# Kernel optimization log

Measured on AMD Instinct MI355X. Metric: run time of the kernel, lower is better.

Reference implementation:

```python
import jax, jax.numpy as jnp
import numpy as np

N, C, H, W = 8, 256, 128, 128
HW = H * W
NB = 20            # boxes per image
TEMP = 0.5
RATIO = 1.0
IMG_H, IMG_W = 800.0, 800.0  # img_metas[i]['img_shape']


def setup_inputs() -> dict:
    key = jax.random.key(0)
    k1, k2, k3 = jax.random.split(key, 3)
    preds_S = jax.random.normal(k1, (HW, N, C), dtype=jnp.float32)
    preds_T = jax.random.normal(k2, (HW, N, C), dtype=jnp.float32)
    # boxes: random corner pairs in image coords, sorted so x1<=x2, y1<=y2
    u = jax.random.uniform(k3, (N, NB, 4), dtype=jnp.float32)
    x1 = jnp.minimum(u[..., 0], u[..., 2]) * IMG_W
    x2 = jnp.maximum(u[..., 0], u[..., 2]) * IMG_W
    y1 = jnp.minimum(u[..., 1], u[..., 3]) * IMG_H
    y2 = jnp.maximum(u[..., 1], u[..., 3]) * IMG_H
    gt_bboxes = jnp.stack([x1, y1, x2, y2], axis=-1)  # (N, NB, 4)
    return {"preds_S": preds_S, "preds_T": preds_T, "gt_bboxes": gt_bboxes}


def get_attention(preds, temp):
    # preds: (N, C, H, W)
    value = jnp.abs(preds)
    fea_map = value.mean(axis=1)                                   # (N, H, W)
    S_att = (H * W) * jax.nn.softmax((fea_map / temp).reshape(N, -1), axis=1)
    S_att = S_att.reshape(N, H, W)
    channel_map = value.mean(axis=(2, 3))                          # (N, C)
    C_att = C * jax.nn.softmax(channel_map / temp, axis=1)
    return S_att, C_att


def build_masks(gt_bboxes):
    # boxes scaled to feature grid (same math as torch loop, vectorized)
    wmin = jnp.floor(gt_bboxes[..., 0] / IMG_W * W).astype(jnp.int32)  # (N, NB)
    wmax = jnp.ceil(gt_bboxes[..., 2] / IMG_W * W).astype(jnp.int32)
    hmin = jnp.floor(gt_bboxes[..., 1] / IMG_H * H).astype(jnp.int32)
    hmax = jnp.ceil(gt_bboxes[..., 3] / IMG_H * H).astype(jnp.int32)
    area = 1.0 / (hmax + 1 - hmin).astype(jnp.float32) / (wmax + 1 - wmin).astype(jnp.float32)
    hh = jnp.arange(H)[None, None, :, None]
    ww = jnp.arange(W)[None, None, None, :]
    inside = ((hh >= hmin[:, :, None, None]) & (hh <= hmax[:, :, None, None]) &
              (ww >= wmin[:, :, None, None]) & (ww <= wmax[:, :, None, None]))  # (N, NB, H, W)
    # per-box max-scatter == max over boxes of (area where inside else 0)
    Mask_fg = jnp.max(jnp.where(inside, area[:, :, None, None], 0.0), axis=1)  # (N, H, W)
    Mask_bg = (Mask_fg <= 0).astype(jnp.float32)
    s = Mask_bg.sum(axis=(1, 2), keepdims=True)
    Mask_bg = jnp.where(s > 0, Mask_bg / s, Mask_bg)
    return Mask_fg, Mask_bg


def reference(preds_S, preds_T, gt_bboxes):
    # attention from DETACHED teacher features (preds_T.detach() in torch)
    pT_det = jax.lax.stop_gradient(preds_T)
    pT_new = pT_det.reshape(H, W, N, C).transpose(2, 3, 0, 1)  # (N, C, H, W)
    S_t, C_t = get_attention(pT_new, TEMP)

    Mask_fg, Mask_bg = build_masks(gt_bboxes)

    # flatten to the (HW, bs, .) layout of get_fea_loss
    flat = lambda m: m.transpose(1, 2, 0).reshape(HW, N, 1)
    S_t_f = flat(S_t)
    Mfg_f = flat(Mask_fg)
    Mbg_f = flat(Mask_bg)
    C_t_f = C_t[None]  # (1, bs, c) broadcast

    w = jnp.sqrt(S_t_f) * jnp.sqrt(C_t_f)
    fea_t = preds_T * w
    fea_s = preds_S * w
    diff = jnp.abs(fea_s - fea_t)
    fg_loss = jnp.sum(diff * jnp.sqrt(Mfg_f)) / HW
    bg_loss = jnp.sum(diff * jnp.sqrt(Mbg_f)) / HW
    return (fg_loss + bg_loss) * RATIO
```

## Files before the change

### kernel.cpp

```cpp
#include <hip/hip_runtime.h>

#define N_   8
#define C_   256
#define H_   128
#define W_   128
#define HW_  16384
#define NB_  20
constexpr float TEMP  = 0.5f;
constexpr float IMG_W = 800.0f;
constexpr float IMG_H = 800.0f;

using f4 = __attribute__((ext_vector_type(4))) float;

__device__ __forceinline__ float waveReduceSum(float v) {
    v += __shfl_xor(v, 32, 64);
    v += __shfl_xor(v, 16, 64);
    v += __shfl_xor(v, 8, 64);
    v += __shfl_xor(v, 4, 64);
    v += __shfl_xor(v, 2, 64);
    v += __shfl_xor(v, 1, 64);
    return v;
}

__global__ __launch_bounds__(256, 4) void k_stats(const float* __restrict__ pT,
                                                  float* __restrict__ chan_part,
                                                  float* __restrict__ fea_sum,
                                                  float* __restrict__ smax_part) {
    const int n     = blockIdx.x & 7;
    const int chunk = blockIdx.x >> 3;
    const int wave  = threadIdx.x >> 6;
    const int lane  = threadIdx.x & 63;
    const int hw0   = chunk * 64 + wave * 16;

    float4 cacc = make_float4(0.f, 0.f, 0.f, 0.f);
    float vmax = 0.f;
    #pragma unroll
    for (int g = 0; g < 4; ++g) {
        const int r = hw0 + g * 4;
        float p[4];
        #pragma unroll
        for (int j = 0; j < 4; ++j) {
            const float4 v = *(const float4*)(pT + ((size_t)((r + j) * N_ + n)) * C_ + lane * 4);
            const float ax = fabsf(v.x), ay = fabsf(v.y), az = fabsf(v.z), aw = fabsf(v.w);
            cacc.x += ax; cacc.y += ay; cacc.z += az; cacc.w += aw;
            p[j] = ax + ay + az + aw;
        }
        float a01 = (lane & 32) ? p[1] : p[0];
        float b01 = (lane & 32) ? p[0] : p[1];
        const float u01 = a01 + __shfl_xor(b01, 32, 64);
        float a23 = (lane & 32) ? p[3] : p[2];
        float b23 = (lane & 32) ? p[2] : p[3];
        const float u23 = a23 + __shfl_xor(b23, 32, 64);
        float aq = (lane & 16) ? u23 : u01;
        float bq = (lane & 16) ? u01 : u23;
        float u = aq + __shfl_xor(bq, 16, 64);
        u += __shfl_xor(u, 8, 64);
        u += __shfl_xor(u, 4, 64);
        u += __shfl_xor(u, 2, 64);
        u += __shfl_xor(u, 1, 64);
        vmax = fmaxf(vmax, u);
        if ((lane & 15) == 0) {
            const int q = lane >> 4;
            const int row = ((q & 1) << 1) | (q >> 1);
            fea_sum[n * HW_ + r + row] = u;
        }
    }
    vmax = fmaxf(vmax, __shfl_xor(vmax, 16, 64));
    vmax = fmaxf(vmax, __shfl_xor(vmax, 32, 64));

    __shared__ float lds[4][C_];
    __shared__ float wmax[4];
    if (lane == 0) wmax[wave] = vmax;
    ((float4*)lds[wave])[lane] = cacc;
    __syncthreads();
    const int c = threadIdx.x;
    chan_part[((size_t)(n * 256 + chunk)) * C_ + c] =
        lds[0][c] + lds[1][c] + lds[2][c] + lds[3][c];
    if (threadIdx.x == 0)
        smax_part[n * 256 + chunk] =
            fmaxf(fmaxf(wmax[0], wmax[1]), fmaxf(wmax[2], wmax[3]));
}

__global__ __launch_bounds__(256) void k_prep(const float* __restrict__ fea_sum,
                                              const float* __restrict__ chan_part,
                                              const float* __restrict__ smax_part,
                                              const float* __restrict__ gt,
                                              float* __restrict__ A_t,
                                              float* __restrict__ B) {
    const int n   = blockIdx.x >> 3;
    const int sub = blockIdx.x & 7;
    const int tid = threadIdx.x;
    __shared__ float red[256];
    __shared__ int   bb[NB_][4];
    __shared__ float barea[NB_];

    if (tid < NB_) {
        const float* bx = gt + ((size_t)n * NB_ + tid) * 4;
        const int wmin = (int)floorf(bx[0] / IMG_W * (float)W_);
        const int wmax = (int)ceilf (bx[2] / IMG_W * (float)W_);
        const int hmin = (int)floorf(bx[1] / IMG_H * (float)H_);
        const int hmax = (int)ceilf (bx[3] / IMG_H * (float)H_);
        bb[tid][0] = wmin; bb[tid][1] = wmax; bb[tid][2] = hmin; bb[tid][3] = hmax;
        barea[tid] = 1.0f / (float)(hmax + 1 - hmin) / (float)(wmax + 1 - wmin);
    }

    red[tid] = smax_part[n * 256 + tid];
    __syncthreads();
    for (int s = 128; s > 0; s >>= 1) { if (tid < s) red[tid] = fmaxf(red[tid], red[tid + s]); __syncthreads(); }
    const float sm = red[0] * (1.0f / (C_ * TEMP));
    __syncthreads();

    float acc = 0.f;
    for (int i = tid; i < HW_; i += 256)
        acc += expf(fea_sum[n * HW_ + i] * (1.0f / (C_ * TEMP)) - sm);
    red[tid] = acc; __syncthreads();
    for (int s = 128; s > 0; s >>= 1) { if (tid < s) red[tid] += red[tid + s]; __syncthreads(); }
    const float sden = red[0];
    __syncthreads();

    float cnt = 0.f;
    for (int i = tid; i < HW_; i += 256) {
        const int h = i >> 7, w = i & 127;
        bool in = false;
        for (int b = 0; b < NB_; ++b)
            in = in || (h >= bb[b][2] && h <= bb[b][3] && w >= bb[b][0] && w <= bb[b][1]);
        cnt += in ? 0.f : 1.f;
    }
    red[tid] = cnt; __syncthreads();
    for (int s = 128; s > 0; s >>= 1) { if (tid < s) red[tid] += red[tid + s]; __syncthreads(); }
    const float bgs = red[0];
    const float bginv = (bgs > 0.f) ? 1.0f / bgs : 1.0f;
    __syncthreads();

    for (int k = 0; k < 8; ++k) {
        const int i = sub * 2048 + k * 256 + tid;
        const int h = i >> 7, w = i & 127;
        float fg = 0.f;
        for (int b = 0; b < NB_; ++b)
            if (h >= bb[b][2] && h <= bb[b][3] && w >= bb[b][0] && w <= bb[b][1])
                fg = fmaxf(fg, barea[b]);
        const float S_att = (float)HW_ * expf(fea_sum[n * HW_ + i] * (1.0f / (C_ * TEMP)) - sm) / sden;
        const float bg = (fg <= 0.f) ? bginv : 0.f;
        A_t[(size_t)i * 8 + n] = sqrtf(S_att) * (sqrtf(fg) + sqrtf(bg)) * (1.0f / (float)HW_);
    }

    if (sub != 0) return;
    __syncthreads();

    float cs = 0.f;
    #pragma unroll 4
    for (int k2 = 0; k2 < 256; ++k2)
        cs += chan_part[((size_t)(n * 256 + k2)) * C_ + tid];
    const float lc = cs * (1.0f / (HW_ * TEMP));
    red[tid] = lc; __syncthreads();
    for (int s = 128; s > 0; s >>= 1) { if (tid < s) red[tid] = fmaxf(red[tid], red[tid + s]); __syncthreads(); }
    const float cmax = red[0]; __syncthreads();
    const float e = expf(lc - cmax);
    red[tid] = e; __syncthreads();
    for (int s = 128; s > 0; s >>= 1) { if (tid < s) red[tid] += red[tid + s]; __syncthreads(); }
    B[n * C_ + tid] = sqrtf((float)C_ * e / red[0]);
}

__global__ __launch_bounds__(256, 4) void k_main(const float* __restrict__ pS,
                                                 const float* __restrict__ pT,
                                                 const float* __restrict__ A_t,
                                                 const float* __restrict__ B,
                                                 float* __restrict__ partials) {
    __shared__ float4 ldsB[512];
    const int tid = threadIdx.x;
    ldsB[tid]       = ((const float4*)B)[tid];
    ldsB[tid + 256] = ((const float4*)B)[tid + 256];
    __syncthreads();

    const int wave = tid >> 6, lane = tid & 63;
    const int hw   = blockIdx.x * 4 + wave;
    float a[8];
    #pragma unroll
    for (int j = 0; j < 8; ++j) a[j] = A_t[(size_t)hw * 8 + j];

    const size_t base4 = (size_t)hw * 512 + lane;
    f4 sv[8], tv[8];
    #pragma unroll
    for (int j = 0; j < 8; ++j) {
        sv[j] = __builtin_nontemporal_load((const f4*)pS + base4 + (size_t)j * 64);
        tv[j] = *((const f4*)pT + base4 + (size_t)j * 64);
    }
    float acc = 0.f;
    #pragma unroll
    for (int j = 0; j < 8; ++j) {
        const float4 b4 = ldsB[j * 64 + lane];
        const float part = fabsf(sv[j].x - tv[j].x) * b4.x + fabsf(sv[j].y - tv[j].y) * b4.y +
                           fabsf(sv[j].z - tv[j].z) * b4.z + fabsf(sv[j].w - tv[j].w) * b4.w;
        acc += a[j] * part;
    }
    acc = waveReduceSum(acc);
    __shared__ float red[4];
    if (lane == 0) red[wave] = acc;
    __syncthreads();
    if (tid == 0) partials[blockIdx.x] = red[0] + red[1] + red[2] + red[3];
}

__global__ __launch_bounds__(256) void k_final(const float* __restrict__ partials,
                                               float* __restrict__ out) {
    float a = 0.f;
    for (int i = threadIdx.x; i < 4096; i += 256) a += partials[i];
    __shared__ float red[256];
    red[threadIdx.x] = a; __syncthreads();
    for (int s = 128; s > 0; s >>= 1) { if (threadIdx.x < s) red[threadIdx.x] += red[threadIdx.x + s]; __syncthreads(); }
    if (threadIdx.x == 0) out[0] = red[0];
}

extern "C" void kernel_launch(void* const* d_in, const int* in_sizes, int n_in,
                              void* d_out, int out_size, void* d_ws, size_t ws_size,
                              hipStream_t stream) {
    const float* pS = (const float*)d_in[0];
    const float* pT = (const float*)d_in[1];
    const float* gt = (const float*)d_in[2];
    float* ws = (float*)d_ws;

    float* chan_part = ws;
    float* smax_part = chan_part + 524288;
    float* fea_sum   = smax_part + 2048;
    float* A_t       = fea_sum + 131072;
    float* B         = A_t + 131072;
    float* partials  = B + 2048;

    k_stats<<<2048, 256, 0, stream>>>(pT, chan_part, fea_sum, smax_part);
    k_prep <<<64,   256, 0, stream>>>(fea_sum, chan_part, smax_part, gt, A_t, B);
    k_main <<<4096, 256, 0, stream>>>(pS, pT, A_t, B, partials);
    k_final<<<1,    256, 0, stream>>>(partials, (float*)d_out);
}
```

Baseline: 384.7 us.

## Read teacher rows contiguously in stats kernel and split prep reductions across more blocks

The stats kernel now has each wave load 16 consecutive 1 KB rows (two spatial positions across all eight images) instead of eight scattered rows per image, accumulating per-image channel sums in registers. The single-pass prep kernel is split into a 256-block kernel that computes partial softmax denominators, background counts and channel sub-sums, followed by a 64-block kernel that finishes the reductions and writes the weights. This aims to give coalesced, high-ILP loads in the stats pass and to remove the serial tail of the 64-block prep kernel. In exchange, the channel partial buffer grows eightfold (16 MB of extra writes and reads) and there is one more kernel launch.

```diff
diff --git a/kernel.cpp b/kernel.cpp
--- a/kernel.cpp
+++ b/kernel.cpp
@@ -26,30 +26,37 @@
                                                   float* __restrict__ chan_part,
                                                   float* __restrict__ fea_sum,
                                                   float* __restrict__ smax_part) {
-    const int n     = blockIdx.x & 7;
-    const int chunk = blockIdx.x >> 3;
-    const int wave  = threadIdx.x >> 6;
-    const int lane  = threadIdx.x & 63;
-    const int hw0   = chunk * 64 + wave * 16;
-
-    float4 cacc = make_float4(0.f, 0.f, 0.f, 0.f);
-    float vmax = 0.f;
+    const int bid  = blockIdx.x;
+    const int wave = threadIdx.x >> 6;
+    const int lane = threadIdx.x & 63;
+    const int hw0  = bid * 8 + wave * 2;
+    const int row0 = hw0 * 8;
+
+    float4 v[16];
+    #pragma unroll
+    for (int j = 0; j < 16; ++j)
+        v[j] = *(const float4*)(pT + ((size_t)(row0 + j)) * C_ + lane * 4);
+
+    float4 cacc[8];
+    float p[16];
+    #pragma unroll
+    for (int j = 0; j < 16; ++j) {
+        const float ax = fabsf(v[j].x), ay = fabsf(v[j].y), az = fabsf(v[j].z), aw = fabsf(v[j].w);
+        p[j] = ax + ay + az + aw;
+        const int n = j & 7;
+        if (j < 8) cacc[n] = make_float4(ax, ay, az, aw);
+        else { cacc[n].x += ax; cacc[n].y += ay; cacc[n].z += az; cacc[n].w += aw; }
+    }
+
+    float vlo = 0.f, vhi = 0.f;
     #pragma unroll
     for (int g = 0; g < 4; ++g) {
-        const int r = hw0 + g * 4;
-        float p[4];
-        #pragma unroll
-        for (int j = 0; j < 4; ++j) {
-            const float4 v = *(const float4*)(pT + ((size_t)((r + j) * N_ + n)) * C_ + lane * 4);
-            const float ax = fabsf(v.x), ay = fabsf(v.y), az = fabsf(v.z), aw = fabsf(v.w);
-            cacc.x += ax; cacc.y += ay; cacc.z += az; cacc.w += aw;
-            p[j] = ax + ay + az + aw;
-        }
-        float a01 = (lane & 32) ? p[1] : p[0];
-        float b01 = (lane & 32) ? p[0] : p[1];
+        const float p0 = p[g*4+0], p1 = p[g*4+1], p2 = p[g*4+2], p3 = p[g*4+3];
+        float a01 = (lane & 32) ? p1 : p0;
+        float b01 = (lane & 32) ? p0 : p1;
         const float u01 = a01 + __shfl_xor(b01, 32, 64);
-        float a23 = (lane & 32) ? p[3] : p[2];
-        float b23 = (lane & 32) ? p[2] : p[3];
+        float a23 = (lane & 32) ? p3 : p2;
+        float b23 = (lane & 32) ? p2 : p3;
         const float u23 = a23 + __shfl_xor(b23, 32, 64);
         float aq = (lane & 16) ? u23 : u01;
         float bq = (lane & 16) ? u01 : u23;
@@ -58,41 +65,112 @@
         u += __shfl_xor(u, 4, 64);
         u += __shfl_xor(u, 2, 64);
         u += __shfl_xor(u, 1, 64);
-        vmax = fmaxf(vmax, u);
+        if (g & 1) vhi = fmaxf(vhi, u); else vlo = fmaxf(vlo, u);
         if ((lane & 15) == 0) {
-            const int q = lane >> 4;
-            const int row = ((q & 1) << 1) | (q >> 1);
-            fea_sum[n * HW_ + r + row] = u;
+            const int q  = lane >> 4;
+            const int j  = g * 4 + (((q & 1) << 1) | (q >> 1));
+            fea_sum[(j & 7) * HW_ + hw0 + (j >> 3)] = u;
         }
     }
-    vmax = fmaxf(vmax, __shfl_xor(vmax, 16, 64));
-    vmax = fmaxf(vmax, __shfl_xor(vmax, 32, 64));
-
-    __shared__ float lds[4][C_];
-    __shared__ float wmax[4];
-    if (lane == 0) wmax[wave] = vmax;
-    ((float4*)lds[wave])[lane] = cacc;
-    __syncthreads();
-    const int c = threadIdx.x;
-    chan_part[((size_t)(n * 256 + chunk)) * C_ + c] =
-        lds[0][c] + lds[1][c] + lds[2][c] + lds[3][c];
-    if (threadIdx.x == 0)
-        smax_part[n * 256 + chunk] =
-            fmaxf(fmaxf(wmax[0], wmax[1]), fmaxf(wmax[2], wmax[3]));
-}
-
-__global__ __launch_bounds__(256) void k_prep(const float* __restrict__ fea_sum,
+
+    __shared__ float ldsc[4][8][C_];
+    __shared__ float wmax[4][8];
+    if ((lane & 15) == 0) {
+        const int q   = lane >> 4;
+        const int nlo = ((q & 1) << 1) | (q >> 1);
+        wmax[wave][nlo]     = vlo;
+        wmax[wave][nlo + 4] = vhi;
+    }
+    #pragma unroll
+    for (int n = 0; n < 8; ++n)
+        *(float4*)&ldsc[wave][n][lane * 4] = cacc[n];
+    __syncthreads();
+    const int tid = threadIdx.x;
+    #pragma unroll
+    for (int n = 0; n < 8; ++n) {
+        const float s = ldsc[0][n][tid] + ldsc[1][n][tid] + ldsc[2][n][tid] + ldsc[3][n][tid];
+        chan_part[((size_t)n * 2048 + bid) * C_ + tid] = s;
+    }
+    if (tid < 8)
+        smax_part[tid * 2048 + bid] =
+            fmaxf(fmaxf(wmax[0][tid], wmax[1][tid]), fmaxf(wmax[2][tid], wmax[3][tid]));
+}
+
+__global__ __launch_bounds__(256) void k_soft(const float* __restrict__ fea_sum,
                                               const float* __restrict__ chan_part,
                                               const float* __restrict__ smax_part,
                                               const float* __restrict__ gt,
-                                              float* __restrict__ A_t,
-                                              float* __restrict__ B) {
+                                              float* __restrict__ sden_part,
+                                              float* __restrict__ bg_part,
+                                              float* __restrict__ chan_sub,
+                                              float* __restrict__ stats) {
+    const int n   = blockIdx.x >> 5;
+    const int sub = blockIdx.x & 31;
+    const int tid = threadIdx.x;
+    __shared__ float red[256];
+    __shared__ int   bb[NB_][4];
+
+    if (tid < NB_) {
+        const float* bx = gt + ((size_t)n * NB_ + tid) * 4;
+        bb[tid][0] = (int)floorf(bx[0] / IMG_W * (float)W_);
+        bb[tid][1] = (int)ceilf (bx[2] / IMG_W * (float)W_);
+        bb[tid][2] = (int)floorf(bx[1] / IMG_H * (float)H_);
+        bb[tid][3] = (int)ceilf (bx[3] / IMG_H * (float)H_);
+    }
+
+    float m = -1e30f;
+    #pragma unroll
+    for (int k = 0; k < 8; ++k) m = fmaxf(m, smax_part[n * 2048 + k * 256 + tid]);
+    red[tid] = m; __syncthreads();
+    for (int s = 128; s > 0; s >>= 1) { if (tid < s) red[tid] = fmaxf(red[tid], red[tid + s]); __syncthreads(); }
+    const float sm = red[0] * (1.0f / (C_ * TEMP));
+    __syncthreads();
+
+    float acc = 0.f;
+    #pragma unroll
+    for (int k = 0; k < 2; ++k)
+        acc += expf(fea_sum[n * HW_ + sub * 512 + k * 256 + tid] * (1.0f / (C_ * TEMP)) - sm);
+    red[tid] = acc; __syncthreads();
+    for (int s = 128; s > 0; s >>= 1) { if (tid < s) red[tid] += red[tid + s]; __syncthreads(); }
+    if (tid == 0) sden_part[n * 32 + sub] = red[0];
+    __syncthreads();
+
+    float cnt = 0.f;
+    #pragma unroll
+    for (int k = 0; k < 2; ++k) {
+        const int i = sub * 512 + k * 256 + tid;
+        const int h = i >> 7, w = i & 127;
+        bool in = false;
+        for (int b = 0; b < NB_; ++b)
+            in = in || (h >= bb[b][2] && h <= bb[b][3] && w >= bb[b][0] && w <= bb[b][1]);
+        cnt += in ? 0.f : 1.f;
+    }
+    red[tid] = cnt; __syncthreads();
+    for (int s = 128; s > 0; s >>= 1) { if (tid < s) red[tid] += red[tid + s]; __syncthreads(); }
+    if (tid == 0) bg_part[n * 32 + sub] = red[0];
+    if (tid == 0 && sub == 0) stats[n] = sm;
+
+    float cs = 0.f;
+    #pragma unroll 4
+    for (int k = 0; k < 64; ++k)
+        cs += chan_part[((size_t)n * 2048 + sub * 64 + k) * C_ + tid];
+    chan_sub[((size_t)n * 32 + sub) * C_ + tid] = cs;
+}
+
+__global__ __launch_bounds__(256) void k_A(const float* __restrict__ fea_sum,
+                                           const float* __restrict__ gt,
+                                           const float* __restrict__ sden_part,
+                                           const float* __restrict__ bg_part,
+                                           const float* __restrict__ stats,
+                                           const float* __restrict__ chan_sub,
+                                           float* __restrict__ A_t,
+                                           float* __restrict__ B) {
     const int n   = blockIdx.x >> 3;
     const int sub = blockIdx.x & 7;
     const int tid = threadIdx.x;
-    __shared__ float red[256];
     __shared__ int   bb[NB_][4];
     __shared__ float barea[NB_];
+    __shared__ float red[256];
 
     if (tid < NB_) {
         const float* bx = gt + ((size_t)n * NB_ + tid) * 4;
@@ -103,35 +181,14 @@
         bb[tid][0] = wmin; bb[tid][1] = wmax; bb[tid][2] = hmin; bb[tid][3] = hmax;
         barea[tid] = 1.0f / (float)(hmax + 1 - hmin) / (float)(wmax + 1 - wmin);
     }
-
-    red[tid] = smax_part[n * 256 + tid];
-    __syncthreads();
-    for (int s = 128; s > 0; s >>= 1) { if (tid < s) red[tid] = fmaxf(red[tid], red[tid + s]); __syncthreads(); }
-    const float sm = red[0] * (1.0f / (C_ * TEMP));
-    __syncthreads();
-
-    float acc = 0.f;
-    for (int i = tid; i < HW_; i += 256)
-        acc += expf(fea_sum[n * HW_ + i] * (1.0f / (C_ * TEMP)) - sm);
-    red[tid] = acc; __syncthreads();
-    for (int s = 128; s > 0; s >>= 1) { if (tid < s) red[tid] += red[tid + s]; __syncthreads(); }
-    const float sden = red[0];
-    __syncthreads();
-
-    float cnt = 0.f;
-    for (int i = tid; i < HW_; i += 256) {
-        const int h = i >> 7, w = i & 127;
-        bool in = false;
-        for (int b = 0; b < NB_; ++b)
-            in = in || (h >= bb[b][2] && h <= bb[b][3] && w >= bb[b][0] && w <= bb[b][1]);
-        cnt += in ? 0.f : 1.f;
-    }
-    red[tid] = cnt; __syncthreads();
-    for (int s = 128; s > 0; s >>= 1) { if (tid < s) red[tid] += red[tid + s]; __syncthreads(); }
-    const float bgs = red[0];
+    const float sm = stats[n];
+    float sden = 0.f, bgs = 0.f;
+    #pragma unroll
+    for (int j = 0; j < 32; ++j) { sden += sden_part[n * 32 + j]; bgs += bg_part[n * 32 + j]; }
     const float bginv = (bgs > 0.f) ? 1.0f / bgs : 1.0f;
     __syncthreads();
 
+    #pragma unroll
     for (int k = 0; k < 8; ++k) {
         const int i = sub * 2048 + k * 256 + tid;
         const int h = i >> 7, w = i & 127;
@@ -146,11 +203,10 @@
 
     if (sub != 0) return;
     __syncthreads();
-
     float cs = 0.f;
-    #pragma unroll 4
-    for (int k2 = 0; k2 < 256; ++k2)
-        cs += chan_part[((size_t)(n * 256 + k2)) * C_ + tid];
+    #pragma unroll
+    for (int s = 0; s < 32; ++s)
+        cs += chan_sub[((size_t)n * 32 + s) * C_ + tid];
     const float lc = cs * (1.0f / (HW_ * TEMP));
     red[tid] = lc; __syncthreads();
     for (int s = 128; s > 0; s >>= 1) { if (tid < s) red[tid] = fmaxf(red[tid], red[tid + s]); __syncthreads(); }
@@ -219,14 +275,21 @@
     float* ws = (float*)d_ws;
 
     float* chan_part = ws;
-    float* smax_part = chan_part + 524288;
-    float* fea_sum   = smax_part + 2048;
+    float* smax_part = chan_part + 4194304;
+    float* sden_part = smax_part + 16384;
+    float* bg_part   = sden_part + 256;
+    float* stats     = bg_part + 256;
+    float* chan_sub  = stats + 16;
+    float* fea_sum   = chan_sub + 65536;
     float* A_t       = fea_sum + 131072;
     float* B         = A_t + 131072;
     float* partials  = B + 2048;
 
     k_stats<<<2048, 256, 0, stream>>>(pT, chan_part, fea_sum, smax_part);
-    k_prep <<<64,   256, 0, stream>>>(fea_sum, chan_part, smax_part, gt, A_t, B);
+    k_soft <<<256,  256, 0, stream>>>(fea_sum, chan_part, smax_part, gt,
+                                      sden_part, bg_part, chan_sub, stats);
+    k_A    <<<64,   256, 0, stream>>>(fea_sum, gt, sden_part, bg_part, stats,
+                                      chan_sub, A_t, B);
     k_main <<<4096, 256, 0, stream>>>(pS, pT, A_t, B, partials);
     k_final<<<1,    256, 0, stream>>>(partials, (float*)d_out);
 }
```

New measurement: 319.6 us. -16.9%, faster.
